# Kernel tuning notes

Measured on AMD Instinct MI355X. Metric: run time of the kernel, lower is better.

The kernel has to match this reference:

```python
import jax, jax.numpy as jnp
import numpy as np

SQ, B, NP, HN = 2048, 2, 16, 64  # [seq, batch, heads, head_dim]

def setup_inputs() -> dict:
    key = jax.random.key(0)
    kq, kk, kv = jax.random.split(key, 3)
    return {
        "query": jax.random.normal(kq, (SQ, B, NP, HN), dtype=jnp.float32),
        "key":   jax.random.normal(kk, (SQ, B, NP, HN), dtype=jnp.float32),
        "value": jax.random.normal(kv, (SQ, B, NP, HN), dtype=jnp.float32),
    }

def reference(query, key, value):
    sq, b, nheads, hn = query.shape
    # NOTE: original module computes norm_factor=sqrt(hn) but never applies it;
    # scores are UNscaled QK^T, replicated faithfully here.
    scores = jnp.einsum('sbnh,tbnh->bnst', query, key)          # [b, np, sq, sk]
    probs = jax.nn.softmax(scores, axis=-1)                      # mask=None -> plain softmax
    # dropout is deterministic (train=False default) -> identity
    context = jnp.einsum('bnst,tbnh->sbnh', probs, value)        # [sq, b, np, hn]
    return context.reshape(sq, b, nheads * hn).astype(jnp.float32)
```

## Files before the change

### kernel.cpp

```cpp
#include <hip/hip_runtime.h>
#include <math.h>
#include <stdint.h>

#define SQ 2048
#define NBH 32
#define HN 64
#define BQ 128
#define BK 64
#define BK2 128
#define NP2 (SQ/BK2)
#define TOK 2048
#define HSTRIDE (SQ*HN)

typedef _Float16 half2v __attribute__((ext_vector_type(2)));
typedef _Float16 half4v __attribute__((ext_vector_type(4)));
typedef _Float16 half8v __attribute__((ext_vector_type(8)));
typedef float f32x16 __attribute__((ext_vector_type(16)));

__device__ __forceinline__ void async16(const void* g, void* l) {
  __builtin_amdgcn_global_load_lds(
      (const __attribute__((address_space(1))) void*)g,
      (__attribute__((address_space(3))) void*)l, 16, 0, 0);
}

__device__ __forceinline__ float fexp2(float x) {
#if __has_builtin(__builtin_amdgcn_exp2f)
  return __builtin_amdgcn_exp2f(x);
#else
  return exp2f(x);
#endif
}

__global__ __launch_bounds__(256) void prep_kv(const float* __restrict__ K,
                                               const float* __restrict__ V,
                                               _Float16* __restrict__ Kh,
                                               _Float16* __restrict__ Vt) {
  __shared__ _Float16 vs[HN * 64];
  const int t = threadIdx.x;
  const int head = blockIdx.y;
  {
    const int key = blockIdx.x * 64 + (t >> 2);
    const int c0 = (t & 3) * 2;
    const float* src = K + (size_t)key * TOK + head * HN + c0 * 8;
    float4 a = *(const float4*)src;
    float4 b = *(const float4*)(src + 4);
    float4 c = *(const float4*)(src + 8);
    float4 d = *(const float4*)(src + 12);
    half8v h0, h1;
    h0[0]=(_Float16)a.x; h0[1]=(_Float16)a.y; h0[2]=(_Float16)a.z; h0[3]=(_Float16)a.w;
    h0[4]=(_Float16)b.x; h0[5]=(_Float16)b.y; h0[6]=(_Float16)b.z; h0[7]=(_Float16)b.w;
    h1[0]=(_Float16)c.x; h1[1]=(_Float16)c.y; h1[2]=(_Float16)c.z; h1[3]=(_Float16)c.w;
    h1[4]=(_Float16)d.x; h1[5]=(_Float16)d.y; h1[6]=(_Float16)d.z; h1[7]=(_Float16)d.w;
    _Float16* row = Kh + (size_t)head * HSTRIDE + (size_t)key * 64;
    *(half8v*)&row[((c0    ) ^ (key & 7)) * 8] = h0;
    *(half8v*)&row[((c0 + 1) ^ (key & 7)) * 8] = h1;
  }
  {
    const int kt = blockIdx.x * 64;
    const int kl = (t >> 3) * 2;
    const int db = (t & 7) * 8;
    const float* src = V + (size_t)(kt + kl) * TOK + head * HN + db;
    float4 a0 = *(const float4*)src;
    float4 a1 = *(const float4*)(src + 4);
    float4 b0 = *(const float4*)(src + TOK);
    float4 b1 = *(const float4*)(src + TOK + 4);
    const float av[8] = {a0.x,a0.y,a0.z,a0.w,a1.x,a1.y,a1.z,a1.w};
    const float bv[8] = {b0.x,b0.y,b0.z,b0.w,b1.x,b1.y,b1.z,b1.w};
    const int u = kl >> 2;
    #pragma unroll
    for (int j = 0; j < 8; ++j) {
      const int dim = db + j;
      const int pos = u ^ (dim & 15);
      half2v h; h[0] = (_Float16)av[j]; h[1] = (_Float16)bv[j];
      *(half2v*)&vs[dim * 64 + pos * 4 + (kl & 3)] = h;
    }
    __syncthreads();
    const int dim = t >> 2;
    const int q = (t & 3) ^ (dim & 3);
    const _Float16* srow = &vs[dim * 64 + q * 16];
    _Float16* drow = Vt + (size_t)head * HSTRIDE + (size_t)dim * SQ + kt + q * 16;
    *(half8v*)&drow[0] = *(const half8v*)&srow[0];
    *(half8v*)&drow[8] = *(const half8v*)&srow[8];
  }
}

__global__ __launch_bounds__(256, 2)
void fattn_mfma(const float* __restrict__ Q, const _Float16* __restrict__ Kh,
                const _Float16* __restrict__ Vt, float* __restrict__ O) {
  __shared__ __align__(16) _Float16 kbf[2][2 * BK * 64];
  __shared__ __align__(16) _Float16 vtf[2][2 * HN * 64];

  const int t = threadIdx.x;
  const int lane = t & 63;
  const int w = t >> 6;
  const int h2 = lane >> 5;
  const int l31 = lane & 31;
  const int q0 = blockIdx.x * BQ + w * 32;
  const int head = blockIdx.y;
  const _Float16* Kp = Kh + (size_t)head * HSTRIDE;
  const _Float16* Vp = Vt + (size_t)head * HSTRIDE;

  half8v qf[4];
  {
    const float* qp = Q + (size_t)(q0 + l31) * TOK + head * HN + 8 * h2;
    const float s = 1.44269504088896f;
    #pragma unroll
    for (int ks = 0; ks < 4; ++ks) {
      float4 a = *(const float4*)(qp + 16 * ks);
      float4 b = *(const float4*)(qp + 16 * ks + 4);
      half8v f;
      f[0] = (_Float16)(s*a.x); f[1] = (_Float16)(s*a.y); f[2] = (_Float16)(s*a.z); f[3] = (_Float16)(s*a.w);
      f[4] = (_Float16)(s*b.x); f[5] = (_Float16)(s*b.y); f[6] = (_Float16)(s*b.z); f[7] = (_Float16)(s*b.w);
      qf[ks] = f;
    }
  }

  f32x16 acc0, acc1;
  #pragma unroll
  for (int r = 0; r < 16; ++r) { acc0[r] = 0.f; acc1[r] = 0.f; }
  float m_i = -INFINITY, l_i = 0.f;

  auto stage = [&](int p) {
    const int buf = p & 1;
    const size_t kt = (size_t)p * BK2;
    #pragma unroll
    for (int i = 0; i < 4; ++i) {
      const int off = w * 512 + i * 2048;
      async16(Kp + kt * 64 + off + lane * 8, &kbf[buf][off]);
    }
    #pragma unroll
    for (int tl = 0; tl < 2; ++tl)
      #pragma unroll
      for (int i = 0; i < 2; ++i) {
        const int off = w * 1024 + i * 512;
        const int eo = off + lane * 8;
        const int dim = eo >> 6, inner = eo & 63;
        async16(Vp + (size_t)dim * SQ + kt + tl * 64 + inner,
                &vtf[buf][tl * 4096 + off]);
      }
  };

  stage(0);
  for (int p = 0; p < NP2; ++p) {
    __syncthreads();
    if (p + 1 < NP2) stage(p + 1);
    const int cur = p & 1;

    f32x16 sa0, sa1, sb0, sb1;
    {
      f32x16 c0, c1, d0, d1;
      #pragma unroll
      for (int r = 0; r < 16; ++r) { c0[r]=0.f; c1[r]=0.f; d0[r]=0.f; d1[r]=0.f; }
      #pragma unroll
      for (int ks = 0; ks < 4; ++ks) {
        const int pos = ((h2 + 2 * ks) ^ (l31 & 7)) * 8;
        half8v a0v = *(const half8v*)&kbf[cur][l31 * 64 + pos];
        half8v a1v = *(const half8v*)&kbf[cur][(l31 + 32) * 64 + pos];
        half8v b0v = *(const half8v*)&kbf[cur][4096 + l31 * 64 + pos];
        half8v b1v = *(const half8v*)&kbf[cur][4096 + (l31 + 32) * 64 + pos];
        c0 = __builtin_amdgcn_mfma_f32_32x32x16_f16(a0v, qf[ks], c0, 0, 0, 0);
        c1 = __builtin_amdgcn_mfma_f32_32x32x16_f16(a1v, qf[ks], c1, 0, 0, 0);
        d0 = __builtin_amdgcn_mfma_f32_32x32x16_f16(b0v, qf[ks], d0, 0, 0, 0);
        d1 = __builtin_amdgcn_mfma_f32_32x32x16_f16(b1v, qf[ks], d1, 0, 0, 0);
      }
      sa0 = c0; sa1 = c1; sb0 = d0; sb1 = d1;
    }

    float mx = -INFINITY;
    #pragma unroll
    for (int r = 0; r < 16; ++r)
      mx = fmaxf(mx, fmaxf(fmaxf(sa0[r], sa1[r]), fmaxf(sb0[r], sb1[r])));
    mx = fmaxf(mx, __shfl_xor(mx, 32, 64));
    const float mnew = fmaxf(m_i, mx);
    const float alpha = fexp2(m_i - mnew);
    float rsum = 0.f;
    #pragma unroll
    for (int r = 0; r < 16; ++r) {
      float p0 = fexp2(sa0[r] - mnew);
      float p1 = fexp2(sa1[r] - mnew);
      float p2 = fexp2(sb0[r] - mnew);
      float p3 = fexp2(sb1[r] - mnew);
      sa0[r] = p0; sa1[r] = p1; sb0[r] = p2; sb1[r] = p3;
      rsum += (p0 + p1) + (p2 + p3);
    }
    rsum += __shfl_xor(rsum, 32, 64);
    l_i = l_i * alpha + rsum;
    m_i = mnew;
    #pragma unroll
    for (int r = 0; r < 16; ++r) { acc0[r] *= alpha; acc1[r] *= alpha; }

    #pragma unroll
    for (int tl = 0; tl < 2; ++tl) {
      const int vbase = tl * 4096;
      #pragma unroll
      for (int ks = 0; ks < 4; ++ks) {
        const int rb = 8 * (ks & 1);
        const f32x16& s = tl ? ((ks < 2) ? sb0 : sb1) : ((ks < 2) ? sa0 : sa1);
        union { half8v v8; half2v v2[4]; } pu;
        #pragma unroll
        for (int tt = 0; tt < 4; ++tt) {
          auto pk = __builtin_amdgcn_cvt_pkrtz(s[rb + 2 * tt], s[rb + 2 * tt + 1]);
          pu.v2[tt] = *(half2v*)&pk;
        }
        #pragma unroll
        for (int mbd = 0; mbd < 2; ++mbd) {
          const int dim = l31 + 32 * mbd;
          const int sw = dim & 15;
          union { half8v v8; half4v v4[2]; } au;
          au.v4[0] = *(const half4v*)&vtf[cur][vbase + dim * 64 + ((4 * ks + h2)     ^ sw) * 4];
          au.v4[1] = *(const half4v*)&vtf[cur][vbase + dim * 64 + ((4 * ks + 2 + h2) ^ sw) * 4];
          if (mbd == 0)
            acc0 = __builtin_amdgcn_mfma_f32_32x32x16_f16(au.v8, pu.v8, acc0, 0, 0, 0);
          else
            acc1 = __builtin_amdgcn_mfma_f32_32x32x16_f16(au.v8, pu.v8, acc1, 0, 0, 0);
        }
      }
    }
  }

  const float invl = 1.f / l_i;
  float* orow = O + (size_t)(q0 + l31) * TOK + head * HN;
  #pragma unroll
  for (int r = 0; r < 16; ++r) {
    const int d = (r & 3) + 8 * (r >> 2) + 4 * h2;
    orow[d]      = acc0[r] * invl;
    orow[d + 32] = acc1[r] * invl;
  }
}

extern "C" void kernel_launch(void* const* d_in, const int* in_sizes, int n_in,
                              void* d_out, int out_size, void* d_ws, size_t ws_size,
                              hipStream_t stream) {
  const float* Q = (const float*)d_in[0];
  const float* K = (const float*)d_in[1];
  const float* V = (const float*)d_in[2];
  float* O = (float*)d_out;
  _Float16* Kh = (_Float16*)d_ws;
  _Float16* Vh = Kh + (size_t)NBH * HSTRIDE;
  prep_kv<<<dim3(SQ / 64, NBH), 256, 0, stream>>>(K, V, Kh, Vh);
  fattn_mfma<<<dim3(SQ / BQ, NBH), 256, 0, stream>>>(Q, Kh, Vh, O);
}
```

Baseline: 142.8 us.

## Switch attention to 16x16x32 MFMA with direct-global K reads and pre-tiled V

Rewrites the attention kernel to use 16x16x32 MFMA tiles with 16 queries per wave and 64 per block, raising occupancy hints to 4 blocks per CU. K is now read directly from global memory into registers instead of being staged through LDS, and the log2e scale moves from Q into the K prep kernel. V is pre-tiled by the prep kernel into contiguous swizzled 8K-element tiles so each stage is a single linear async copy. The changes aim to cut LDS traffic and raise parallelism, at the cost of heavier global and L2 traffic for K and less K reuse per block.

```diff
diff --git a/kernel.cpp b/kernel.cpp
--- a/kernel.cpp
+++ b/kernel.cpp
@@ -1,28 +1,25 @@
 #include <hip/hip_runtime.h>
 #include <math.h>
-#include <stdint.h>
 
 #define SQ 2048
 #define NBH 32
 #define HN 64
-#define BQ 128
-#define BK 64
+#define BQ 64
+#define QW 16
 #define BK2 128
-#define NP2 (SQ/BK2)
+#define NPH2 16
 #define TOK 2048
-#define HSTRIDE (SQ*HN)
+#define VTILE 8192
 
 typedef _Float16 half2v __attribute__((ext_vector_type(2)));
-typedef _Float16 half4v __attribute__((ext_vector_type(4)));
 typedef _Float16 half8v __attribute__((ext_vector_type(8)));
-typedef float f32x16 __attribute__((ext_vector_type(16)));
+typedef float f32x4 __attribute__((ext_vector_type(4)));
 
 __device__ __forceinline__ void async16(const void* g, void* l) {
   __builtin_amdgcn_global_load_lds(
       (const __attribute__((address_space(1))) void*)g,
       (__attribute__((address_space(3))) void*)l, 16, 0, 0);
 }
-
 __device__ __forceinline__ float fexp2(float x) {
 #if __has_builtin(__builtin_amdgcn_exp2f)
   return __builtin_amdgcn_exp2f(x);
@@ -35,197 +32,172 @@
                                                const float* __restrict__ V,
                                                _Float16* __restrict__ Kh,
                                                _Float16* __restrict__ Vt) {
-  __shared__ _Float16 vs[HN * 64];
+  __shared__ _Float16 vs[VTILE];
   const int t = threadIdx.x;
   const int head = blockIdx.y;
+  const int kt0 = blockIdx.x * 128;
+  const float LOG2E = 1.44269504088896f;
   {
-    const int key = blockIdx.x * 64 + (t >> 2);
-    const int c0 = (t & 3) * 2;
-    const float* src = K + (size_t)key * TOK + head * HN + c0 * 8;
-    float4 a = *(const float4*)src;
-    float4 b = *(const float4*)(src + 4);
-    float4 c = *(const float4*)(src + 8);
-    float4 d = *(const float4*)(src + 12);
-    half8v h0, h1;
-    h0[0]=(_Float16)a.x; h0[1]=(_Float16)a.y; h0[2]=(_Float16)a.z; h0[3]=(_Float16)a.w;
-    h0[4]=(_Float16)b.x; h0[5]=(_Float16)b.y; h0[6]=(_Float16)b.z; h0[7]=(_Float16)b.w;
-    h1[0]=(_Float16)c.x; h1[1]=(_Float16)c.y; h1[2]=(_Float16)c.z; h1[3]=(_Float16)c.w;
-    h1[4]=(_Float16)d.x; h1[5]=(_Float16)d.y; h1[6]=(_Float16)d.z; h1[7]=(_Float16)d.w;
-    _Float16* row = Kh + (size_t)head * HSTRIDE + (size_t)key * 64;
-    *(half8v*)&row[((c0    ) ^ (key & 7)) * 8] = h0;
-    *(half8v*)&row[((c0 + 1) ^ (key & 7)) * 8] = h1;
-  }
-  {
-    const int kt = blockIdx.x * 64;
-    const int kl = (t >> 3) * 2;
-    const int db = (t & 7) * 8;
-    const float* src = V + (size_t)(kt + kl) * TOK + head * HN + db;
+    const int key = kt0 + (t >> 1);
+    const int d0 = (t & 1) * 32;
+    const float* src = K + (size_t)key * TOK + head * HN + d0;
+    _Float16* dst = Kh + ((size_t)head * SQ + key) * HN + d0;
+    #pragma unroll
+    for (int i = 0; i < 4; ++i) {
+      float4 a = *(const float4*)(src + i * 8);
+      float4 b = *(const float4*)(src + i * 8 + 4);
+      half8v h;
+      h[0]=(_Float16)(LOG2E*a.x); h[1]=(_Float16)(LOG2E*a.y);
+      h[2]=(_Float16)(LOG2E*a.z); h[3]=(_Float16)(LOG2E*a.w);
+      h[4]=(_Float16)(LOG2E*b.x); h[5]=(_Float16)(LOG2E*b.y);
+      h[6]=(_Float16)(LOG2E*b.z); h[7]=(_Float16)(LOG2E*b.w);
+      *(half8v*)(dst + i * 8) = h;
+    }
+  }
+  #pragma unroll
+  for (int tau = 0; tau < 2; ++tau) {
+    const int task = t + tau * 256;
+    const int k2 = (task & 63) * 2;
+    const int db = (task >> 6) * 8;
+    const float* src = V + (size_t)(kt0 + k2) * TOK + head * HN + db;
     float4 a0 = *(const float4*)src;
     float4 a1 = *(const float4*)(src + 4);
     float4 b0 = *(const float4*)(src + TOK);
     float4 b1 = *(const float4*)(src + TOK + 4);
     const float av[8] = {a0.x,a0.y,a0.z,a0.w,a1.x,a1.y,a1.z,a1.w};
     const float bv[8] = {b0.x,b0.y,b0.z,b0.w,b1.x,b1.y,b1.z,b1.w};
-    const int u = kl >> 2;
+    const int ks = k2 >> 5, gg = (k2 >> 2) & 3, hh = (k2 >> 4) & 1, r = k2 & 3;
     #pragma unroll
     for (int j = 0; j < 8; ++j) {
-      const int dim = db + j;
-      const int pos = u ^ (dim & 15);
+      const int d = db + j;
+      const int pos = (4 * ks + gg) ^ (d & 15);
       half2v h; h[0] = (_Float16)av[j]; h[1] = (_Float16)bv[j];
-      *(half2v*)&vs[dim * 64 + pos * 4 + (kl & 3)] = h;
-    }
-    __syncthreads();
-    const int dim = t >> 2;
-    const int q = (t & 3) ^ (dim & 3);
-    const _Float16* srow = &vs[dim * 64 + q * 16];
-    _Float16* drow = Vt + (size_t)head * HSTRIDE + (size_t)dim * SQ + kt + q * 16;
-    *(half8v*)&drow[0] = *(const half8v*)&srow[0];
-    *(half8v*)&drow[8] = *(const half8v*)&srow[8];
-  }
-}
-
-__global__ __launch_bounds__(256, 2)
+      *(half2v*)&vs[d * 128 + pos * 8 + hh * 4 + r] = h;
+    }
+  }
+  __syncthreads();
+  _Float16* dst = Vt + ((size_t)head * NPH2 + blockIdx.x) * VTILE;
+  #pragma unroll
+  for (int i = 0; i < 4; ++i) {
+    const int idx = i * 256 + t;
+    *(half8v*)(dst + idx * 8) = *(const half8v*)&vs[idx * 8];
+  }
+}
+
+__global__ __launch_bounds__(256, 4)
 void fattn_mfma(const float* __restrict__ Q, const _Float16* __restrict__ Kh,
                 const _Float16* __restrict__ Vt, float* __restrict__ O) {
-  __shared__ __align__(16) _Float16 kbf[2][2 * BK * 64];
-  __shared__ __align__(16) _Float16 vtf[2][2 * HN * 64];
-
+  __shared__ __align__(16) _Float16 vtf[2][VTILE];
   const int t = threadIdx.x;
   const int lane = t & 63;
   const int w = t >> 6;
-  const int h2 = lane >> 5;
-  const int l31 = lane & 31;
-  const int q0 = blockIdx.x * BQ + w * 32;
+  const int n = lane & 15;
+  const int g = lane >> 4;
+  const int qb = blockIdx.x * BQ + w * QW;
   const int head = blockIdx.y;
-  const _Float16* Kp = Kh + (size_t)head * HSTRIDE;
-  const _Float16* Vp = Vt + (size_t)head * HSTRIDE;
-
-  half8v qf[4];
+  const _Float16* Kp = Kh + (size_t)head * SQ * HN;
+  const _Float16* Vp = Vt + (size_t)head * NPH2 * VTILE;
+
+  half8v qf[2];
   {
-    const float* qp = Q + (size_t)(q0 + l31) * TOK + head * HN + 8 * h2;
-    const float s = 1.44269504088896f;
-    #pragma unroll
-    for (int ks = 0; ks < 4; ++ks) {
-      float4 a = *(const float4*)(qp + 16 * ks);
-      float4 b = *(const float4*)(qp + 16 * ks + 4);
+    const float* qp = Q + (size_t)(qb + n) * TOK + head * HN + 8 * g;
+    #pragma unroll
+    for (int ks = 0; ks < 2; ++ks) {
+      float4 a = *(const float4*)(qp + 32 * ks);
+      float4 b = *(const float4*)(qp + 32 * ks + 4);
       half8v f;
-      f[0] = (_Float16)(s*a.x); f[1] = (_Float16)(s*a.y); f[2] = (_Float16)(s*a.z); f[3] = (_Float16)(s*a.w);
-      f[4] = (_Float16)(s*b.x); f[5] = (_Float16)(s*b.y); f[6] = (_Float16)(s*b.z); f[7] = (_Float16)(s*b.w);
+      f[0]=(_Float16)a.x; f[1]=(_Float16)a.y; f[2]=(_Float16)a.z; f[3]=(_Float16)a.w;
+      f[4]=(_Float16)b.x; f[5]=(_Float16)b.y; f[6]=(_Float16)b.z; f[7]=(_Float16)b.w;
       qf[ks] = f;
     }
   }
 
-  f32x16 acc0, acc1;
-  #pragma unroll
-  for (int r = 0; r < 16; ++r) { acc0[r] = 0.f; acc1[r] = 0.f; }
+  f32x4 acc[4];
+  #pragma unroll
+  for (int dt = 0; dt < 4; ++dt) acc[dt] = (f32x4){0.f, 0.f, 0.f, 0.f};
   float m_i = -INFINITY, l_i = 0.f;
 
   auto stage = [&](int p) {
-    const int buf = p & 1;
-    const size_t kt = (size_t)p * BK2;
+    const _Float16* src = Vp + (size_t)p * VTILE;
     #pragma unroll
     for (int i = 0; i < 4; ++i) {
-      const int off = w * 512 + i * 2048;
-      async16(Kp + kt * 64 + off + lane * 8, &kbf[buf][off]);
-    }
-    #pragma unroll
-    for (int tl = 0; tl < 2; ++tl)
+      const int idx = i * 256 + t;
+      async16(src + idx * 8, &vtf[p & 1][idx * 8]);
+    }
+  };
+
+  stage(0);
+  for (int p = 0; p < NPH2; ++p) {
+    __syncthreads();
+    if (p + 1 < NPH2) stage(p + 1);
+    const int cur = p & 1;
+
+    f32x4 sf[8];
+    #pragma unroll
+    for (int ks = 0; ks < 2; ++ks) {
+      half8v kf[8];
       #pragma unroll
-      for (int i = 0; i < 2; ++i) {
-        const int off = w * 1024 + i * 512;
-        const int eo = off + lane * 8;
-        const int dim = eo >> 6, inner = eo & 63;
-        async16(Vp + (size_t)dim * SQ + kt + tl * 64 + inner,
-                &vtf[buf][tl * 4096 + off]);
+      for (int kt = 0; kt < 8; ++kt)
+        kf[kt] = *(const half8v*)(Kp + (size_t)(p * BK2 + kt * 16 + n) * HN +
+                                  32 * ks + 8 * g);
+      #pragma unroll
+      for (int kt = 0; kt < 8; ++kt) {
+        f32x4 c = (ks == 0) ? (f32x4){0.f, 0.f, 0.f, 0.f} : sf[kt];
+        sf[kt] = __builtin_amdgcn_mfma_f32_16x16x32_f16(kf[kt], qf[ks], c, 0, 0, 0);
       }
-  };
-
-  stage(0);
-  for (int p = 0; p < NP2; ++p) {
-    __syncthreads();
-    if (p + 1 < NP2) stage(p + 1);
-    const int cur = p & 1;
-
-    f32x16 sa0, sa1, sb0, sb1;
-    {
-      f32x16 c0, c1, d0, d1;
-      #pragma unroll
-      for (int r = 0; r < 16; ++r) { c0[r]=0.f; c1[r]=0.f; d0[r]=0.f; d1[r]=0.f; }
-      #pragma unroll
-      for (int ks = 0; ks < 4; ++ks) {
-        const int pos = ((h2 + 2 * ks) ^ (l31 & 7)) * 8;
-        half8v a0v = *(const half8v*)&kbf[cur][l31 * 64 + pos];
-        half8v a1v = *(const half8v*)&kbf[cur][(l31 + 32) * 64 + pos];
-        half8v b0v = *(const half8v*)&kbf[cur][4096 + l31 * 64 + pos];
-        half8v b1v = *(const half8v*)&kbf[cur][4096 + (l31 + 32) * 64 + pos];
-        c0 = __builtin_amdgcn_mfma_f32_32x32x16_f16(a0v, qf[ks], c0, 0, 0, 0);
-        c1 = __builtin_amdgcn_mfma_f32_32x32x16_f16(a1v, qf[ks], c1, 0, 0, 0);
-        d0 = __builtin_amdgcn_mfma_f32_32x32x16_f16(b0v, qf[ks], d0, 0, 0, 0);
-        d1 = __builtin_amdgcn_mfma_f32_32x32x16_f16(b1v, qf[ks], d1, 0, 0, 0);
-      }
-      sa0 = c0; sa1 = c1; sb0 = d0; sb1 = d1;
     }
 
     float mx = -INFINITY;
     #pragma unroll
-    for (int r = 0; r < 16; ++r)
-      mx = fmaxf(mx, fmaxf(fmaxf(sa0[r], sa1[r]), fmaxf(sb0[r], sb1[r])));
+    for (int kt = 0; kt < 8; ++kt)
+      mx = fmaxf(mx, fmaxf(fmaxf(sf[kt][0], sf[kt][1]), fmaxf(sf[kt][2], sf[kt][3])));
+    mx = fmaxf(mx, __shfl_xor(mx, 16, 64));
     mx = fmaxf(mx, __shfl_xor(mx, 32, 64));
     const float mnew = fmaxf(m_i, mx);
     const float alpha = fexp2(m_i - mnew);
     float rsum = 0.f;
     #pragma unroll
-    for (int r = 0; r < 16; ++r) {
-      float p0 = fexp2(sa0[r] - mnew);
-      float p1 = fexp2(sa1[r] - mnew);
-      float p2 = fexp2(sb0[r] - mnew);
-      float p3 = fexp2(sb1[r] - mnew);
-      sa0[r] = p0; sa1[r] = p1; sb0[r] = p2; sb1[r] = p3;
+    for (int kt = 0; kt < 8; ++kt) {
+      float p0 = fexp2(sf[kt][0] - mnew);
+      float p1 = fexp2(sf[kt][1] - mnew);
+      float p2 = fexp2(sf[kt][2] - mnew);
+      float p3 = fexp2(sf[kt][3] - mnew);
+      sf[kt][0] = p0; sf[kt][1] = p1; sf[kt][2] = p2; sf[kt][3] = p3;
       rsum += (p0 + p1) + (p2 + p3);
     }
+    rsum += __shfl_xor(rsum, 16, 64);
     rsum += __shfl_xor(rsum, 32, 64);
     l_i = l_i * alpha + rsum;
     m_i = mnew;
     #pragma unroll
-    for (int r = 0; r < 16; ++r) { acc0[r] *= alpha; acc1[r] *= alpha; }
-
-    #pragma unroll
-    for (int tl = 0; tl < 2; ++tl) {
-      const int vbase = tl * 4096;
+    for (int dt = 0; dt < 4; ++dt) acc[dt] *= alpha;
+
+    #pragma unroll
+    for (int ks = 0; ks < 4; ++ks) {
+      union { half8v v8; half2v v2[4]; } pu;
+      auto c0 = __builtin_amdgcn_cvt_pkrtz(sf[2*ks][0],   sf[2*ks][1]);
+      auto c1 = __builtin_amdgcn_cvt_pkrtz(sf[2*ks][2],   sf[2*ks][3]);
+      auto c2 = __builtin_amdgcn_cvt_pkrtz(sf[2*ks+1][0], sf[2*ks+1][1]);
+      auto c3 = __builtin_amdgcn_cvt_pkrtz(sf[2*ks+1][2], sf[2*ks+1][3]);
+      pu.v2[0] = *(half2v*)&c0; pu.v2[1] = *(half2v*)&c1;
+      pu.v2[2] = *(half2v*)&c2; pu.v2[3] = *(half2v*)&c3;
+      const int pos = (4 * ks + g) ^ n;
+      const _Float16* vb = &vtf[cur][n * 128 + pos * 8];
       #pragma unroll
-      for (int ks = 0; ks < 4; ++ks) {
-        const int rb = 8 * (ks & 1);
-        const f32x16& s = tl ? ((ks < 2) ? sb0 : sb1) : ((ks < 2) ? sa0 : sa1);
-        union { half8v v8; half2v v2[4]; } pu;
-        #pragma unroll
-        for (int tt = 0; tt < 4; ++tt) {
-          auto pk = __builtin_amdgcn_cvt_pkrtz(s[rb + 2 * tt], s[rb + 2 * tt + 1]);
-          pu.v2[tt] = *(half2v*)&pk;
-        }
-        #pragma unroll
-        for (int mbd = 0; mbd < 2; ++mbd) {
-          const int dim = l31 + 32 * mbd;
-          const int sw = dim & 15;
-          union { half8v v8; half4v v4[2]; } au;
-          au.v4[0] = *(const half4v*)&vtf[cur][vbase + dim * 64 + ((4 * ks + h2)     ^ sw) * 4];
-          au.v4[1] = *(const half4v*)&vtf[cur][vbase + dim * 64 + ((4 * ks + 2 + h2) ^ sw) * 4];
-          if (mbd == 0)
-            acc0 = __builtin_amdgcn_mfma_f32_32x32x16_f16(au.v8, pu.v8, acc0, 0, 0, 0);
-          else
-            acc1 = __builtin_amdgcn_mfma_f32_32x32x16_f16(au.v8, pu.v8, acc1, 0, 0, 0);
-        }
+      for (int dt = 0; dt < 4; ++dt) {
+        half8v av = *(const half8v*)(vb + dt * 2048);
+        acc[dt] = __builtin_amdgcn_mfma_f32_16x16x32_f16(av, pu.v8, acc[dt], 0, 0, 0);
       }
     }
   }
 
   const float invl = 1.f / l_i;
-  float* orow = O + (size_t)(q0 + l31) * TOK + head * HN;
-  #pragma unroll
-  for (int r = 0; r < 16; ++r) {
-    const int d = (r & 3) + 8 * (r >> 2) + 4 * h2;
-    orow[d]      = acc0[r] * invl;
-    orow[d + 32] = acc1[r] * invl;
-  }
+  float* orow = O + (size_t)(qb + n) * TOK + head * HN;
+  #pragma unroll
+  for (int dt = 0; dt < 4; ++dt)
+    #pragma unroll
+    for (int r = 0; r < 4; ++r)
+      orow[16 * dt + 4 * g + r] = acc[dt][r] * invl;
 }
 
 extern "C" void kernel_launch(void* const* d_in, const int* in_sizes, int n_in,
@@ -236,7 +208,7 @@
   const float* V = (const float*)d_in[2];
   float* O = (float*)d_out;
   _Float16* Kh = (_Float16*)d_ws;
-  _Float16* Vh = Kh + (size_t)NBH * HSTRIDE;
-  prep_kv<<<dim3(SQ / 64, NBH), 256, 0, stream>>>(K, V, Kh, Vh);
+  _Float16* Vh = Kh + (size_t)NBH * SQ * HN;
+  prep_kv<<<dim3(NPH2, NBH), 256, 0, stream>>>(K, V, Kh, Vh);
   fattn_mfma<<<dim3(SQ / BQ, NBH), 256, 0, stream>>>(Q, Kh, Vh, O);
 }
```

Result: slower. 220.0 us (+54.1%).
